# Kernel tuning notes

Hardware: AMD Instinct MI355X
Metric: run time of the kernel (lower is better)

Reference implementation:

```python
import jax, jax.numpy as jnp
import numpy as np

POOL = (7, 7)
IMAGE_SHAPE = (1024, 1024)  # image_meta image_shape in the original


def setup_inputs() -> dict:
    key = jax.random.key(0)
    ks = jax.random.split(key, 6)
    B, N, C = 2, 1000, 256
    yx = jax.random.uniform(ks[0], (B, N, 2), minval=0.0, maxval=0.7)
    hw = jax.random.uniform(ks[1], (B, N, 2), minval=0.02, maxval=0.3)
    boxes = jnp.concatenate([yx, jnp.clip(yx + hw, 0.0, 1.0)], axis=2)  # (y1,x1,y2,x2) normalized
    sizes = (256, 128, 64, 32)  # strides 4,8,16,32 on a 1024 image
    feats = {f"p{i+2}": jax.random.normal(ks[2 + i], (B, s, s, C), dtype=jnp.float32)
             for i, s in enumerate(sizes)}
    return {"boxes": boxes, **feats}


def _crop_and_resize(feat, boxes, pool_shape):
    # feat: [B,H,W,C], boxes: [B,N,4] normalized (y1,x1,y2,x2)
    B, H, W, C = feat.shape
    ph, pw = pool_shape
    y1, x1, y2, x2 = (boxes[..., i] for i in range(4))
    ty = jnp.linspace(0.0, 1.0, ph)
    tx = jnp.linspace(0.0, 1.0, pw)
    ys = (y1[..., None] + (y2 - y1)[..., None] * ty) * (H - 1)  # [B,N,ph]
    xs = (x1[..., None] + (x2 - x1)[..., None] * tx) * (W - 1)  # [B,N,pw]

    def per_image(f, ys_b, xs_b):
        y0f = jnp.floor(ys_b)
        x0f = jnp.floor(xs_b)
        wy = (ys_b - y0f)[:, :, None, None]  # [N,ph,1,1]
        wx = (xs_b - x0f)[:, None, :, None]  # [N,1,pw,1]
        y0 = jnp.clip(y0f, 0, H - 1).astype(jnp.int32)
        y1i = jnp.clip(y0f + 1, 0, H - 1).astype(jnp.int32)
        x0 = jnp.clip(x0f, 0, W - 1).astype(jnp.int32)
        x1i = jnp.clip(x0f + 1, 0, W - 1).astype(jnp.int32)
        # advanced indexing broadcasts [N,ph,1] x [N,1,pw] -> [N,ph,pw,C]
        v00 = f[y0[:, :, None], x0[:, None, :]]
        v01 = f[y0[:, :, None], x1i[:, None, :]]
        v10 = f[y1i[:, :, None], x0[:, None, :]]
        v11 = f[y1i[:, :, None], x1i[:, None, :]]
        top = v00 + wx * (v01 - v00)
        bot = v10 + wx * (v11 - v10)
        return top + wy * (bot - top)

    return jax.vmap(per_image)(feat, ys, xs)  # [B,N,ph,pw,C]


def reference(boxes, p2, p3, p4, p5):
    feats = (p2, p3, p4, p5)
    y1, x1, y2, x2 = (boxes[..., i] for i in range(4))
    h = y2 - y1
    w = x2 - x1
    image_area = float(IMAGE_SHAPE[0] * IMAGE_SHAPE[1])
    # FPN level assignment: log2(sqrt(hw) / (224/sqrt(area))), clamped to [2,5]
    roi_level = jnp.log2(jnp.sqrt(jnp.maximum(h * w, 1e-12)) / (224.0 / np.sqrt(image_area)))
    roi_level = jnp.clip(jnp.round(roi_level), 2, 5).astype(jnp.int32)  # [B,N]
    out = jnp.zeros(boxes.shape[:2] + POOL + (p2.shape[-1],), dtype=p2.dtype)
    for i, lvl in enumerate(range(2, 6)):
        pooled_l = _crop_and_resize(feats[i], boxes, POOL)  # [B,N,ph,pw,C]
        mask = (roi_level == lvl)[:, :, None, None, None]
        out = out + jnp.where(mask, pooled_l, 0.0)
    return out  # [B,N,ph,pw,C] in original box order
```

## Files before the change

kernel.cpp:

```cpp
#include <hip/hip_runtime.h>


#define NB 2
#define NN 1000
#define NC 256
#define NCELLS (NB * NN * 49)
#define CELLS_PER_WAVE 4
#define WAVES_PER_BLOCK 4
#define CELLS_PER_BLOCK (CELLS_PER_WAVE * WAVES_PER_BLOCK)

typedef float vfloat4 __attribute__((ext_vector_type(4)));

__device__ __forceinline__ void cell_setup(
    int cell,
    const float* __restrict__ boxes,
    const float* __restrict__ p2, const float* __restrict__ p3,
    const float* __restrict__ p4, const float* __restrict__ p5,
    const vfloat4*& a00, const vfloat4*& a01, const vfloat4*& a10, const vfloat4*& a11,
    float& wx, float& wy)
{
    const int pxy = cell % 49;
    const int bn  = cell / 49;
    const int py  = pxy / 7;
    const int px  = pxy % 7;
    const int b   = bn / NN;

    const vfloat4 bx = *(const vfloat4*)(boxes + (size_t)bn * 4);
    const float y1 = bx.x, x1 = bx.y, y2 = bx.z, x2 = bx.w;
    const float h = y2 - y1, w = x2 - x1;

    const float roi = log2f(sqrtf(fmaxf(h * w, 1e-12f)) * (1024.0f / 224.0f));
    int lvl = (int)rintf(roi);
    lvl = min(5, max(2, lvl));

    const float* feat;
    int H;
    switch (lvl) {
        case 2:  feat = p2; H = 256; break;
        case 3:  feat = p3; H = 128; break;
        case 4:  feat = p4; H = 64;  break;
        default: feat = p5; H = 32;  break;
    }
    const int W = H;

    const float ys = (y1 + h * ((float)py * (1.0f / 6.0f))) * (float)(H - 1);
    const float xs = (x1 + w * ((float)px * (1.0f / 6.0f))) * (float)(W - 1);
    const float y0f = floorf(ys), x0f = floorf(xs);
    wy = ys - y0f;
    wx = xs - x0f;
    const int y0 = min(H - 1, max(0, (int)y0f));
    const int yb = min(H - 1, max(0, (int)y0f + 1));
    const int x0 = min(W - 1, max(0, (int)x0f));
    const int xb = min(W - 1, max(0, (int)x0f + 1));

    const size_t base = (size_t)b * H * W * NC;
    a00 = (const vfloat4*)(feat + base + ((size_t)y0 * W + x0) * NC);
    a01 = (const vfloat4*)(feat + base + ((size_t)y0 * W + xb) * NC);
    a10 = (const vfloat4*)(feat + base + ((size_t)yb * W + x0) * NC);
    a11 = (const vfloat4*)(feat + base + ((size_t)yb * W + xb) * NC);
}

__device__ __forceinline__ vfloat4 bilerp4(vfloat4 v00, vfloat4 v01, vfloat4 v10, vfloat4 v11,
                                           float wx, float wy)
{
    vfloat4 top = v00 + wx * (v01 - v00);
    vfloat4 bot = v10 + wx * (v11 - v10);
    return top + wy * (bot - top);
}

__global__ __launch_bounds__(256) void roi_align_kernel(
    const float* __restrict__ boxes,
    const float* __restrict__ p2,
    const float* __restrict__ p3,
    const float* __restrict__ p4,
    const float* __restrict__ p5,
    float* __restrict__ out)
{
    const int lane = threadIdx.x & 63;
    const int wave = threadIdx.x >> 6;

    const int cbase = (blockIdx.x * WAVES_PER_BLOCK + wave) * CELLS_PER_WAVE;

    const vfloat4* a00[CELLS_PER_WAVE];
    const vfloat4* a01[CELLS_PER_WAVE];
    const vfloat4* a10[CELLS_PER_WAVE];
    const vfloat4* a11[CELLS_PER_WAVE];
    float wx[CELLS_PER_WAVE], wy[CELLS_PER_WAVE];

#pragma unroll
    for (int i = 0; i < CELLS_PER_WAVE; ++i) {
        cell_setup(cbase + i, boxes, p2, p3, p4, p5,
                   a00[i], a01[i], a10[i], a11[i], wx[i], wy[i]);
    }

    vfloat4 v00[CELLS_PER_WAVE], v01[CELLS_PER_WAVE], v10[CELLS_PER_WAVE], v11[CELLS_PER_WAVE];
#pragma unroll
    for (int i = 0; i < CELLS_PER_WAVE; ++i) {
        v00[i] = a00[i][lane];
        v01[i] = a01[i][lane];
        v10[i] = a10[i][lane];
        v11[i] = a11[i][lane];
    }

#pragma unroll
    for (int i = 0; i < CELLS_PER_WAVE; ++i) {
        const vfloat4 r = bilerp4(v00[i], v01[i], v10[i], v11[i], wx[i], wy[i]);
        vfloat4* o = (vfloat4*)(out + (size_t)(cbase + i) * NC) + lane;
        __builtin_nontemporal_store(r, o);
    }
}

extern "C" void kernel_launch(void* const* d_in, const int* in_sizes, int n_in,
                              void* d_out, int out_size, void* d_ws, size_t ws_size,
                              hipStream_t stream) {
    const float* boxes = (const float*)d_in[0];
    const float* p2    = (const float*)d_in[1];
    const float* p3    = (const float*)d_in[2];
    const float* p4    = (const float*)d_in[3];
    const float* p5    = (const float*)d_in[4];
    float* out = (float*)d_out;

    const int n_blocks = NCELLS / CELLS_PER_BLOCK;
    roi_align_kernel<<<n_blocks, 256, 0, stream>>>(boxes, p2, p3, p4, p5, out);
}
```

Before: 256.7 us.

## Sort boxes by Morton-binned center and partition cells per XCD for L2 locality

Adds a single-block pre-pass that bins boxes by batch and a 16x16 Morton code of their centers, then builds a permutation with a counting sort. The main kernel becomes a grid-stride loop with a fixed grid of 2048 blocks, and each XCD gets a contiguous range of sorted cells. Spatially nearby boxes therefore share an XCD's L2 and reuse feature-map lines instead of refetching them from HBM. The cost is an extra serial single-block launch plus indirection loads, and the sort only runs when workspace is supplied.

```diff
diff --git a/kernel.cpp b/kernel.cpp
--- a/kernel.cpp
+++ b/kernel.cpp
@@ -3,27 +3,79 @@
 
 #define NB 2
 #define NN 1000
+#define NBOX (NB * NN)
 #define NC 256
-#define NCELLS (NB * NN * 49)
+#define NCELLS (NBOX * 49)
 #define CELLS_PER_WAVE 4
 #define WAVES_PER_BLOCK 4
-#define CELLS_PER_BLOCK (CELLS_PER_WAVE * WAVES_PER_BLOCK)
+#define NBLOCKS 2048
+#define NXCD 8
+#define BLOCKS_PER_XCD (NBLOCKS / NXCD)
+#define WAVES_PER_XCD (BLOCKS_PER_XCD * WAVES_PER_BLOCK)
+#define CELLS_PER_XCD (NCELLS / NXCD)
 
 typedef float vfloat4 __attribute__((ext_vector_type(4)));
 
-__device__ __forceinline__ void cell_setup(
-    int cell,
+__device__ __forceinline__ int box_bin(const float* __restrict__ boxes, int i)
+{
+    const vfloat4 bx = *(const vfloat4*)(boxes + (size_t)i * 4);
+    const float cy = 0.5f * (bx.x + bx.z);
+    const float cx = 0.5f * (bx.y + bx.w);
+    const int yb = min(15, max(0, (int)(cy * 16.0f)));
+    const int xb = min(15, max(0, (int)(cx * 16.0f)));
+    int m = 0;
+#pragma unroll
+    for (int k = 0; k < 4; ++k)
+        m |= (((yb >> k) & 1) << (2 * k + 1)) | (((xb >> k) & 1) << (2 * k));
+    return ((i / NN) << 8) | m;
+}
+
+__global__ __launch_bounds__(256) void sort_boxes_kernel(
+    const float* __restrict__ boxes, int* __restrict__ perm)
+{
+    __shared__ int s_cnt[512];
+    const int tid = threadIdx.x;
+    for (int i = tid; i < 512; i += 256) s_cnt[i] = 0;
+    __syncthreads();
+
+    for (int i = tid; i < NBOX; i += 256)
+        atomicAdd(&s_cnt[box_bin(boxes, i)], 1);
+    __syncthreads();
+
+    if (tid < 64) {
+        int v[8];
+        int part = 0;
+#pragma unroll
+        for (int k = 0; k < 8; ++k) { v[k] = s_cnt[tid * 8 + k]; part += v[k]; }
+        int incl = part;
+#pragma unroll
+        for (int d = 1; d < 64; d <<= 1) {
+            const int n = __shfl_up(incl, d);
+            if (tid >= d) incl += n;
+        }
+        int excl = incl - part;
+#pragma unroll
+        for (int k = 0; k < 8; ++k) { const int t = v[k]; s_cnt[tid * 8 + k] = excl; excl += t; }
+    }
+    __syncthreads();
+
+    for (int i = tid; i < NBOX; i += 256) {
+        const int pos = atomicAdd(&s_cnt[box_bin(boxes, i)], 1);
+        perm[pos] = i;
+    }
+}
+
+__device__ __forceinline__ void cell_setup2(
+    int bn, int pxy,
     const float* __restrict__ boxes,
     const float* __restrict__ p2, const float* __restrict__ p3,
     const float* __restrict__ p4, const float* __restrict__ p5,
     const vfloat4*& a00, const vfloat4*& a01, const vfloat4*& a10, const vfloat4*& a11,
     float& wx, float& wy)
 {
-    const int pxy = cell % 49;
-    const int bn  = cell / 49;
-    const int py  = pxy / 7;
-    const int px  = pxy % 7;
-    const int b   = bn / NN;
+    const int py = pxy / 7;
+    const int px = pxy % 7;
+    const int b  = bn / NN;
 
     const vfloat4 bx = *(const vfloat4*)(boxes + (size_t)bn * 4);
     const float y1 = bx.x, x1 = bx.y, y2 = bx.z, x2 = bx.w;
@@ -74,39 +126,71 @@
     const float* __restrict__ p3,
     const float* __restrict__ p4,
     const float* __restrict__ p5,
+    const int* __restrict__ perm,
     float* __restrict__ out)
 {
     const int lane = threadIdx.x & 63;
     const int wave = threadIdx.x >> 6;
-
-    const int cbase = (blockIdx.x * WAVES_PER_BLOCK + wave) * CELLS_PER_WAVE;
-
-    const vfloat4* a00[CELLS_PER_WAVE];
-    const vfloat4* a01[CELLS_PER_WAVE];
-    const vfloat4* a10[CELLS_PER_WAVE];
-    const vfloat4* a11[CELLS_PER_WAVE];
-    float wx[CELLS_PER_WAVE], wy[CELLS_PER_WAVE];
-
-#pragma unroll
-    for (int i = 0; i < CELLS_PER_WAVE; ++i) {
-        cell_setup(cbase + i, boxes, p2, p3, p4, p5,
-                   a00[i], a01[i], a10[i], a11[i], wx[i], wy[i]);
-    }
-
-    vfloat4 v00[CELLS_PER_WAVE], v01[CELLS_PER_WAVE], v10[CELLS_PER_WAVE], v11[CELLS_PER_WAVE];
-#pragma unroll
-    for (int i = 0; i < CELLS_PER_WAVE; ++i) {
-        v00[i] = a00[i][lane];
-        v01[i] = a01[i][lane];
-        v10[i] = a10[i][lane];
-        v11[i] = a11[i][lane];
-    }
-
-#pragma unroll
-    for (int i = 0; i < CELLS_PER_WAVE; ++i) {
-        const vfloat4 r = bilerp4(v00[i], v01[i], v10[i], v11[i], wx[i], wy[i]);
-        vfloat4* o = (vfloat4*)(out + (size_t)(cbase + i) * NC) + lane;
-        __builtin_nontemporal_store(r, o);
+    const int xcd  = blockIdx.x & (NXCD - 1);
+    const int wl   = (blockIdx.x >> 3) * WAVES_PER_BLOCK + wave;
+    const int start = xcd * CELLS_PER_XCD;
+    const int end   = start + CELLS_PER_XCD;
+
+    for (int base = start + wl * CELLS_PER_WAVE; base < end;
+         base += WAVES_PER_XCD * CELLS_PER_WAVE) {
+
+        if (base + CELLS_PER_WAVE <= end) {
+            const vfloat4* a00[CELLS_PER_WAVE];
+            const vfloat4* a01[CELLS_PER_WAVE];
+            const vfloat4* a10[CELLS_PER_WAVE];
+            const vfloat4* a11[CELLS_PER_WAVE];
+            float wx[CELLS_PER_WAVE], wy[CELLS_PER_WAVE];
+            int ocell[CELLS_PER_WAVE];
+
+#pragma unroll
+            for (int i = 0; i < CELLS_PER_WAVE; ++i) {
+                const int sc  = __builtin_amdgcn_readfirstlane(base + i);
+                const int bns = sc / 49;
+                const int pxy = sc - bns * 49;
+                int bn = perm ? perm[bns] : bns;
+                bn = __builtin_amdgcn_readfirstlane(bn);
+                ocell[i] = bn * 49 + pxy;
+                cell_setup2(bn, pxy, boxes, p2, p3, p4, p5,
+                            a00[i], a01[i], a10[i], a11[i], wx[i], wy[i]);
+            }
+
+            vfloat4 v00[CELLS_PER_WAVE], v01[CELLS_PER_WAVE], v10[CELLS_PER_WAVE], v11[CELLS_PER_WAVE];
+#pragma unroll
+            for (int i = 0; i < CELLS_PER_WAVE; ++i) {
+                v00[i] = a00[i][lane];
+                v01[i] = a01[i][lane];
+                v10[i] = a10[i][lane];
+                v11[i] = a11[i][lane];
+            }
+
+#pragma unroll
+            for (int i = 0; i < CELLS_PER_WAVE; ++i) {
+                const vfloat4 r = bilerp4(v00[i], v01[i], v10[i], v11[i], wx[i], wy[i]);
+                vfloat4* o = (vfloat4*)(out + (size_t)ocell[i] * NC) + lane;
+                __builtin_nontemporal_store(r, o);
+            }
+        } else {
+            for (int i = 0; i < CELLS_PER_WAVE; ++i) {
+                if (base + i >= end) break;
+                const int sc  = __builtin_amdgcn_readfirstlane(base + i);
+                const int bns = sc / 49;
+                const int pxy = sc - bns * 49;
+                int bn = perm ? perm[bns] : bns;
+                bn = __builtin_amdgcn_readfirstlane(bn);
+
+                const vfloat4 *a00, *a01, *a10, *a11;
+                float wx, wy;
+                cell_setup2(bn, pxy, boxes, p2, p3, p4, p5, a00, a01, a10, a11, wx, wy);
+                const vfloat4 r = bilerp4(a00[lane], a01[lane], a10[lane], a11[lane], wx, wy);
+                vfloat4* o = (vfloat4*)(out + (size_t)(bn * 49 + pxy) * NC) + lane;
+                __builtin_nontemporal_store(r, o);
+            }
+        }
     }
 }
 
@@ -120,6 +204,10 @@
     const float* p5    = (const float*)d_in[4];
     float* out = (float*)d_out;
 
-    const int n_blocks = NCELLS / CELLS_PER_BLOCK;
-    roi_align_kernel<<<n_blocks, 256, 0, stream>>>(boxes, p2, p3, p4, p5, out);
-}
+    const int* perm = nullptr;
+    if (d_ws != nullptr && ws_size >= NBOX * sizeof(int)) {
+        sort_boxes_kernel<<<1, 256, 0, stream>>>(boxes, (int*)d_ws);
+        perm = (const int*)d_ws;
+    }
+    roi_align_kernel<<<NBLOCKS, 256, 0, stream>>>(boxes, p2, p3, p4, p5, perm, out);
+}
```

Measured after the change: 266.2 us. +3.7%, slower.
